# Kernel tuning notes

Measured on AMD Instinct MI355X. Metric: run time of the kernel, lower is better.

Reference implementation:

```python
import jax, jax.numpy as jnp
import numpy as np

B, T, IN, H, STEPS = 32768, 11, 2, 64, 80


def gru_cell(x, h, W_ih, W_hh, b_ih, b_hh):
    # PyTorch GRU cell: gates ordered (r, z, n)
    gi = x @ W_ih.T + b_ih            # [B, 3H]
    gh = h @ W_hh.T + b_hh            # [B, 3H]
    gi_r, gi_z, gi_n = jnp.split(gi, 3, axis=-1)
    gh_r, gh_z, gh_n = jnp.split(gh, 3, axis=-1)
    r = jax.nn.sigmoid(gi_r + gh_r)
    z = jax.nn.sigmoid(gi_z + gh_z)
    n = jnp.tanh(gi_n + r * gh_n)
    return (1.0 - z) * n + z * h


def setup_inputs() -> dict:
    key = jax.random.key(0)
    ks = jax.random.split(key, 20)
    s = 1.0 / np.sqrt(H)
    u = lambda k, shape: jax.random.uniform(k, shape, jnp.float32, -s, s)
    inp = {"x": jax.random.normal(ks[0], (B, T, IN), jnp.float32)}
    i = 1
    for pfx, in0 in (("e", IN), ("d", IN)):
        for l, d_in in ((0, in0), (1, H)):
            inp[f"{pfx}W_ih{l}"] = u(ks[i], (3 * H, d_in)); i += 1
            inp[f"{pfx}W_hh{l}"] = u(ks[i], (3 * H, H)); i += 1
            inp[f"{pfx}b_ih{l}"] = u(ks[i], (3 * H,)); i += 1
            inp[f"{pfx}b_hh{l}"] = u(ks[i], (3 * H,)); i += 1
    inp["fc_W"] = u(ks[17], (2, H))
    inp["fc_b"] = u(ks[18], (2,))
    return inp


def reference(x, eW_ih0, eW_hh0, eb_ih0, eb_hh0, eW_ih1, eW_hh1, eb_ih1, eb_hh1,
              dW_ih0, dW_hh0, db_ih0, db_hh0, dW_ih1, dW_hh1, db_ih1, db_hh1,
              fc_W, fc_b):
    b = x.shape[0]
    h0 = jnp.zeros((b, H), x.dtype)
    h1 = jnp.zeros((b, H), x.dtype)

    # ---- encoder: 2-layer GRU over time (dropout inactive in eval) ----
    def enc_step(carry, xt):
        c0, c1 = carry
        c0 = gru_cell(xt, c0, eW_ih0, eW_hh0, eb_ih0, eb_hh0)
        c1 = gru_cell(c0, c1, eW_ih1, eW_hh1, eb_ih1, eb_hh1)
        return (c0, c1), None

    (h0, h1), _ = jax.lax.scan(enc_step, (h0, h1), jnp.swapaxes(x, 0, 1))

    def dec_step(carry, _):
        inp, c0, c1 = carry
        c0 = gru_cell(inp, c0, dW_ih0, dW_hh0, db_ih0, db_hh0)
        c1 = gru_cell(c0, c1, dW_ih1, dW_hh1, db_ih1, db_hh1)
        pred = c1 @ fc_W.T + fc_b     # [B, 2]
        return (pred, c0, c1), pred

    init = (x[:, -1, :], h0, h1)
    _, preds = jax.lax.scan(dec_step, init, None, length=STEPS)  # [80, B, 2]
    return jnp.swapaxes(preds, 0, 1)  # [B, 80, 2]
```

## Files before the change

kernel.cpp:

```cpp
#include <hip/hip_runtime.h>
#include <cstddef>

#define T_SEQ 11
#define STEPS 80

typedef _Float16 f16;
typedef _Float16 f16x4 __attribute__((ext_vector_type(4)));
typedef _Float16 f16x8 __attribute__((ext_vector_type(8)));
typedef float    f32x4 __attribute__((ext_vector_type(4)));

#define SRC (-1.44269504f)
#define SNC ( 2.88539008f)

__device__ __forceinline__ f32x4 mfma16(f16x8 a, f16x8 b, f32x4 c) {
    return __builtin_amdgcn_mfma_f32_16x16x32_f16(a, b, c, 0, 0, 0);
}
__device__ __forceinline__ float exp2r(float x) { return __builtin_amdgcn_exp2f(x); }

__device__ __forceinline__ f16x8 wfrag(const float* __restrict__ W, int row, int k0, float sc) {
    f16x8 r;
    #pragma unroll
    for (int i = 0; i < 8; ++i) r[i] = (f16)(sc * W[row * 64 + k0 + i]);
    return r;
}
__device__ __forceinline__ f16x8 cfrag(const float* __restrict__ Wih0,
                                       const float* __restrict__ fcW, int row, int k0, float sc) {
    f16x8 r;
    #pragma unroll
    for (int i = 0; i < 8; ++i)
        r[i] = (f16)(sc * (Wih0[row * 2] * fcW[k0 + i] + Wih0[row * 2 + 1] * fcW[64 + k0 + i]));
    return r;
}

struct WSet {
    f16x8 xR[2], xZ[2], xN[2];
    f16x8 hR[2], hZ[2], hN[2];
};

__device__ __forceinline__ void load_h_frags(WSet& W, const float* __restrict__ Whh,
                                             int jA, int quad)
{
    #pragma unroll
    for (int ks = 0; ks < 2; ++ks) {
        const int k0 = ks * 32 + quad * 8;
        W.hR[ks] = wfrag(Whh, jA,       k0, SRC);
        W.hZ[ks] = wfrag(Whh, jA + 64,  k0, SRC);
        W.hN[ks] = wfrag(Whh, jA + 128, k0, SNC);
    }
}
__device__ __forceinline__ void load_x_frags(WSet& W, const float* __restrict__ Wx,
                                             int jA, int quad)
{
    #pragma unroll
    for (int ks = 0; ks < 2; ++ks) {
        const int k0 = ks * 32 + quad * 8;
        W.xR[ks] = wfrag(Wx, jA,       k0, SRC);
        W.xZ[ks] = wfrag(Wx, jA + 64,  k0, SRC);
        W.xN[ks] = wfrag(Wx, jA + 128, k0, SNC);
    }
}

template<bool XM, int CT>
__device__ __forceinline__ void cell(const WSet& W, const float* __restrict__ sb,
    const f16* __restrict__ Xs, const f16* __restrict__ Hs, f16* __restrict__ Dst,
    f16x4 (&ho)[2],
    const f32x4* __restrict__ xw, const float2* __restrict__ xv,
    int j4, int ro0, int ro1, int wo)
{
    const f32x4 bR  = *(const f32x4*)(sb + CT * 256 +       j4);
    const f32x4 bZ  = *(const f32x4*)(sb + CT * 256 +  64 + j4);
    const f32x4 bNi = *(const f32x4*)(sb + CT * 256 + 128 + j4);
    const f32x4 bNh = *(const f32x4*)(sb + CT * 256 + 192 + j4);
    #pragma unroll
    for (int mt = 0; mt < 2; ++mt) {
        const int mo = mt * 1024;
        f16x8 hb0 = *(const f16x8*)(Hs + ro0 + mo);
        f16x8 hb1 = *(const f16x8*)(Hs + ro1 + mo);
        f32x4 aR  = mfma16(W.hR[0], hb0, bR);
        f32x4 aZ  = mfma16(W.hZ[0], hb0, bZ);
        f32x4 aNh = mfma16(W.hN[0], hb0, bNh);
        aR  = mfma16(W.hR[1], hb1, aR);
        aZ  = mfma16(W.hZ[1], hb1, aZ);
        aNh = mfma16(W.hN[1], hb1, aNh);
        f32x4 aNi;
        if constexpr (XM) {
            f16x8 xb0 = *(const f16x8*)(Xs + ro0 + mo);
            f16x8 xb1 = *(const f16x8*)(Xs + ro1 + mo);
            aR  = mfma16(W.xR[0], xb0, aR);    aR  = mfma16(W.xR[1], xb1, aR);
            aZ  = mfma16(W.xZ[0], xb0, aZ);    aZ  = mfma16(W.xZ[1], xb1, aZ);
            aNi = mfma16(W.xN[0], xb0, bNi);   aNi = mfma16(W.xN[1], xb1, aNi);
        } else {
            const float x0 = xv[mt].x, x1 = xv[mt].y;
            aR  += x0 * xw[0] + x1 * xw[1];
            aZ  += x0 * xw[2] + x1 * xw[3];
            aNi  = bNi + x0 * xw[4] + x1 * xw[5];
        }
        f16x4 o;
        #pragma unroll
        for (int i = 0; i < 4; ++i) {
            const float r = __builtin_amdgcn_rcpf(1.f + exp2r(aR[i]));
            const float z = __builtin_amdgcn_rcpf(1.f + exp2r(aZ[i]));
            const float n = 1.f - 2.f * __builtin_amdgcn_rcpf(1.f + exp2r(aNi[i] + r * aNh[i]));
            const float h = n + z * ((float)ho[mt][i] - n);
            o[i] = (f16)h;
        }
        ho[mt] = o;
        *(f16x4*)(Dst + wo + mo) = o;
    }
}

__global__ __launch_bounds__(256, 3)
void gru_traj_mfma12(
    const float* __restrict__ x,
    const float* __restrict__ eWih0, const float* __restrict__ eWhh0,
    const float* __restrict__ ebih0, const float* __restrict__ ebhh0,
    const float* __restrict__ eWih1, const float* __restrict__ eWhh1,
    const float* __restrict__ ebih1, const float* __restrict__ ebhh1,
    const float* __restrict__ dWih0, const float* __restrict__ dWhh0,
    const float* __restrict__ dbih0, const float* __restrict__ dbhh0,
    const float* __restrict__ dWih1, const float* __restrict__ dWhh1,
    const float* __restrict__ dbih1, const float* __restrict__ dbhh1,
    const float* __restrict__ fcW,  const float* __restrict__ fcb,
    float* __restrict__ out)
{
    __shared__ f16 hbuf[4][32 * 64];
    __shared__ float2 xe[T_SEQ * 32];
    __shared__ float sbias[4 * 256];
    __shared__ f16 sfc[1024];
    __shared__ float sfcb[2];

    const int tid  = threadIdx.x;
    const int lane = tid & 63;
    const int w    = __builtin_amdgcn_readfirstlane(tid >> 6);
    const int quad = lane >> 4;
    const int col  = lane & 15;
    const int r0   = blockIdx.x * 32;

    {
        const float2* x2 = (const float2*)x;
        for (int i = tid; i < 32 * T_SEQ; i += 256) {
            const int row = i / T_SEQ, t = i - row * T_SEQ;
            xe[t * 32 + row] = x2[(size_t)r0 * T_SEQ + i];
        }
    }
    for (int i = tid; i < 32 * 64; i += 256) { hbuf[0][i] = (f16)0.f; hbuf[2][i] = (f16)0.f; }
    if (tid < 64) {
        const int j = tid;
        sbias[       j] = SRC * (ebih0[j] + ebhh0[j]);
        sbias[ 64 + j] = SRC * (ebih0[64 + j] + ebhh0[64 + j]);
        sbias[128 + j] = SNC * ebih0[128 + j];
        sbias[192 + j] = SNC * ebhh0[128 + j];
        sbias[256 +       j] = SRC * (ebih1[j] + ebhh1[j]);
        sbias[256 +  64 + j] = SRC * (ebih1[64 + j] + ebhh1[64 + j]);
        sbias[256 + 128 + j] = SNC * ebih1[128 + j];
        sbias[256 + 192 + j] = SNC * ebhh1[128 + j];
    }
    for (int e = tid; e < 1024; e += 256) {
        const int ks = e >> 9, rr = e & 511;
        const int lne = rr >> 3, ki = rr & 7;
        const int c = lne & 15, q = lne >> 4;
        const int k = ks * 32 + q * 8 + ki;
        sfc[ks * 512 + lne * 8 + ki] = (c < 2) ? (f16)fcW[c * 64 + k] : (f16)0.f;
    }
    if (tid < 2) sfcb[tid] = fcb[tid];

    const int c7  = col & 7;
    const int ro0 = col * 64 + ((quad ^ c7) << 3);
    const int ro1 = col * 64 + (((4 + quad) ^ c7) << 3);
    const int wo  = col * 64 + ((((w << 1) | (quad >> 1)) ^ c7) << 3) + ((quad & 1) << 2);

    const int jA = w * 16 + col;
    const int j4 = w * 16 + quad * 4;

    f16x4 ho0[2], ho1[2];
    #pragma unroll
    for (int mt = 0; mt < 2; ++mt) {
        #pragma unroll
        for (int i = 0; i < 4; ++i) { ho0[mt][i] = (f16)0.f; ho1[mt][i] = (f16)0.f; }
    }

    WSet W0, W1;
    load_h_frags(W0, eWhh0, jA, quad);
    load_h_frags(W1, eWhh1, jA, quad);
    load_x_frags(W1, eWih1, jA, quad);
    {
        f32x4 xw[6];
        #pragma unroll
        for (int rg = 0; rg < 4; ++rg) {
            xw[0][rg] = SRC * eWih0[(j4 + rg) * 2];        xw[1][rg] = SRC * eWih0[(j4 + rg) * 2 + 1];
            xw[2][rg] = SRC * eWih0[(64 + j4 + rg) * 2];   xw[3][rg] = SRC * eWih0[(64 + j4 + rg) * 2 + 1];
            xw[4][rg] = SNC * eWih0[(128 + j4 + rg) * 2];  xw[5][rg] = SNC * eWih0[(128 + j4 + rg) * 2 + 1];
        }
        __syncthreads();

        #pragma unroll 1
        for (int t = 0; t < T_SEQ - 1; t += 2) {
            float2 xv[2];
            #pragma unroll
            for (int mt = 0; mt < 2; ++mt) xv[mt] = xe[t * 32 + mt * 16 + col];
            cell<false, 0>(W0, sbias, hbuf[0], hbuf[0], hbuf[1], ho0, xw, xv, j4, ro0, ro1, wo);
            __syncthreads();
            cell<true, 1>(W1, sbias, hbuf[1], hbuf[2], hbuf[3], ho1, nullptr, nullptr, j4, ro0, ro1, wo);
            #pragma unroll
            for (int mt = 0; mt < 2; ++mt) xv[mt] = xe[(t + 1) * 32 + mt * 16 + col];
            cell<false, 0>(W0, sbias, hbuf[1], hbuf[1], hbuf[0], ho0, xw, xv, j4, ro0, ro1, wo);
            __syncthreads();
            cell<true, 1>(W1, sbias, hbuf[0], hbuf[3], hbuf[2], ho1, nullptr, nullptr, j4, ro0, ro1, wo);
        }
        {
            float2 xv[2];
            #pragma unroll
            for (int mt = 0; mt < 2; ++mt) xv[mt] = xe[10 * 32 + mt * 16 + col];
            cell<false, 0>(W0, sbias, hbuf[0], hbuf[0], hbuf[1], ho0, xw, xv, j4, ro0, ro1, wo);
            __syncthreads();
            cell<true, 1>(W1, sbias, hbuf[1], hbuf[2], hbuf[3], ho1, nullptr, nullptr, j4, ro0, ro1, wo);
        }
    }

    load_h_frags(W0, dWhh0, jA, quad);
    #pragma unroll
    for (int ks = 0; ks < 2; ++ks) {
        const int k0 = ks * 32 + quad * 8;
        W0.xR[ks] = cfrag(dWih0, fcW, jA,       k0, SRC);
        W0.xZ[ks] = cfrag(dWih0, fcW, jA + 64,  k0, SRC);
        W0.xN[ks] = cfrag(dWih0, fcW, jA + 128, k0, SNC);
    }
    load_h_frags(W1, dWhh1, jA, quad);
    load_x_frags(W1, dWih1, jA, quad);
    if (tid < 64) {
        const int j = tid;
        const float f0 = fcb[0], f1 = fcb[1];
        sbias[512 +       j] = SRC * (dbih0[j] + dbhh0[j] + dWih0[j * 2] * f0 + dWih0[j * 2 + 1] * f1);
        sbias[512 +  64 + j] = SRC * (dbih0[64 + j] + dbhh0[64 + j] + dWih0[(64 + j) * 2] * f0 + dWih0[(64 + j) * 2 + 1] * f1);
        sbias[512 + 128 + j] = SNC * (dbih0[128 + j] + dWih0[(128 + j) * 2] * f0 + dWih0[(128 + j) * 2 + 1] * f1);
        sbias[512 + 192 + j] = SNC * dbhh0[128 + j];
        sbias[768 +       j] = SRC * (dbih1[j] + dbhh1[j]);
        sbias[768 +  64 + j] = SRC * (dbih1[64 + j] + dbhh1[64 + j]);
        sbias[768 + 128 + j] = SNC * dbih1[128 + j];
        sbias[768 + 192 + j] = SNC * dbhh1[128 + j];
    }
    __syncthreads();

    const int cw = w & 1;
    float* __restrict__ op = out + (size_t)(r0 + cw * 16 + col) * (STEPS * 2);

    auto FCout = [&](const f16* h1c) {
        if (w < 2) {
            f32x4 pb;
            const float f0 = sfcb[0], f1 = sfcb[1];
            pb[0] = (quad == 0) ? f0 : 0.f;
            pb[1] = (quad == 0) ? f1 : 0.f;
            pb[2] = 0.f; pb[3] = 0.f;
            f16x8 fc0 = *(const f16x8*)(sfc + lane * 8);
            f16x8 fc1 = *(const f16x8*)(sfc + 512 + lane * 8);
            f16x8 hb0 = *(const f16x8*)(h1c + ro0 + cw * 1024);
            f16x8 hb1 = *(const f16x8*)(h1c + ro1 + cw * 1024);
            f32x4 p = mfma16(fc0, hb0, pb);
            p = mfma16(fc1, hb1, p);
            if (quad == 0) *(float2*)op = make_float2(p[0], p[1]);
        }
        op += 2;
    };

    {
        f32x4 xw[6];
        #pragma unroll
        for (int rg = 0; rg < 4; ++rg) {
            xw[0][rg] = SRC * dWih0[(j4 + rg) * 2];        xw[1][rg] = SRC * dWih0[(j4 + rg) * 2 + 1];
            xw[2][rg] = SRC * dWih0[(64 + j4 + rg) * 2];   xw[3][rg] = SRC * dWih0[(64 + j4 + rg) * 2 + 1];
            xw[4][rg] = SNC * dWih0[(128 + j4 + rg) * 2];  xw[5][rg] = SNC * dWih0[(128 + j4 + rg) * 2 + 1];
        }
        float2 xv0[2];
        #pragma unroll
        for (int mt = 0; mt < 2; ++mt) xv0[mt] = xe[10 * 32 + mt * 16 + col];
        cell<false, 2>(W0, sbias, hbuf[1], hbuf[1], hbuf[0], ho0, xw, xv0, j4, ro0, ro1, wo);
        __syncthreads();
        cell<true, 3>(W1, sbias, hbuf[0], hbuf[3], hbuf[2], ho1, nullptr, nullptr, j4, ro0, ro1, wo);
        __syncthreads();
        FCout(hbuf[2]);
    }

    #pragma unroll 1
    for (int sp = 0; sp < 39; ++sp) {
        cell<true, 2>(W0, sbias, hbuf[2], hbuf[0], hbuf[1], ho0, nullptr, nullptr, j4, ro0, ro1, wo);
        __syncthreads();
        cell<true, 3>(W1, sbias, hbuf[1], hbuf[2], hbuf[3], ho1, nullptr, nullptr, j4, ro0, ro1, wo);
        __syncthreads();
        FCout(hbuf[3]);
        cell<true, 2>(W0, sbias, hbuf[3], hbuf[1], hbuf[0], ho0, nullptr, nullptr, j4, ro0, ro1, wo);
        __syncthreads();
        cell<true, 3>(W1, sbias, hbuf[0], hbuf[3], hbuf[2], ho1, nullptr, nullptr, j4, ro0, ro1, wo);
        __syncthreads();
        FCout(hbuf[2]);
    }
    {
        cell<true, 2>(W0, sbias, hbuf[2], hbuf[0], hbuf[1], ho0, nullptr, nullptr, j4, ro0, ro1, wo);
        __syncthreads();
        cell<true, 3>(W1, sbias, hbuf[1], hbuf[2], hbuf[3], ho1, nullptr, nullptr, j4, ro0, ro1, wo);
        __syncthreads();
        FCout(hbuf[3]);
    }
}

extern "C" void kernel_launch(void* const* d_in, const int* in_sizes, int n_in,
                              void* d_out, int out_size, void* d_ws, size_t ws_size,
                              hipStream_t stream) {
    (void)n_in; (void)out_size; (void)d_ws; (void)ws_size;

    const float* x     = (const float*)d_in[0];
    const float* eWih0 = (const float*)d_in[1];
    const float* eWhh0 = (const float*)d_in[2];
    const float* ebih0 = (const float*)d_in[3];
    const float* ebhh0 = (const float*)d_in[4];
    const float* eWih1 = (const float*)d_in[5];
    const float* eWhh1 = (const float*)d_in[6];
    const float* ebih1 = (const float*)d_in[7];
    const float* ebhh1 = (const float*)d_in[8];
    const float* dWih0 = (const float*)d_in[9];
    const float* dWhh0 = (const float*)d_in[10];
    const float* dbih0 = (const float*)d_in[11];
    const float* dbhh0 = (const float*)d_in[12];
    const float* dWih1 = (const float*)d_in[13];
    const float* dWhh1 = (const float*)d_in[14];
    const float* dbih1 = (const float*)d_in[15];
    const float* dbhh1 = (const float*)d_in[16];
    const float* fcW   = (const float*)d_in[17];
    const float* fcb   = (const float*)d_in[18];
    float* out = (float*)d_out;

    const int b = in_sizes[0] / (T_SEQ * 2);
    dim3 grid(b / 32), block(256);
    hipLaunchKernelGGL(gru_traj_mfma12, grid, block, 0, stream,
        x, eWih0, eWhh0, ebih0, ebhh0, eWih1, eWhh1, ebih1, ebhh1,
        dWih0, dWhh0, dbih0, dbhh0, dWih1, dWhh1, dbih1, dbhh1,
        fcW, fcb, out);
}
```

Measured before the change: 463.6 us.

## Split GRU layers across wave groups and pipeline two row-halves

The block grows from 256 to 512 threads. Waves 0-3 now own layer 0 and waves 4-7 own layer 1, each keeping only one layer's weight fragments in registers. The 32 rows are split into two 16-row halves that move through a software pipeline: layer 1 processes one half while layer 0 processes the other, with double-buffered hidden state in LDS. This aims to halve per-wave register pressure and overlap the two layers' serial dependency chains. The cost is more barriers per step, a larger block, and more complex buffer indexing that could introduce ordering bugs.

```diff
diff --git a/kernel.cpp b/kernel.cpp
--- a/kernel.cpp
+++ b/kernel.cpp
@@ -61,56 +61,50 @@
 }
 
 template<bool XM, int CT>
-__device__ __forceinline__ void cell(const WSet& W, const float* __restrict__ sb,
+__device__ __forceinline__ void cellH(const WSet& W, const float* __restrict__ sb,
     const f16* __restrict__ Xs, const f16* __restrict__ Hs, f16* __restrict__ Dst,
-    f16x4 (&ho)[2],
-    const f32x4* __restrict__ xw, const float2* __restrict__ xv,
+    f16x4& ho, const f32x4* __restrict__ xw, float2 xv,
     int j4, int ro0, int ro1, int wo)
 {
     const f32x4 bR  = *(const f32x4*)(sb + CT * 256 +       j4);
     const f32x4 bZ  = *(const f32x4*)(sb + CT * 256 +  64 + j4);
     const f32x4 bNi = *(const f32x4*)(sb + CT * 256 + 128 + j4);
     const f32x4 bNh = *(const f32x4*)(sb + CT * 256 + 192 + j4);
-    #pragma unroll
-    for (int mt = 0; mt < 2; ++mt) {
-        const int mo = mt * 1024;
-        f16x8 hb0 = *(const f16x8*)(Hs + ro0 + mo);
-        f16x8 hb1 = *(const f16x8*)(Hs + ro1 + mo);
-        f32x4 aR  = mfma16(W.hR[0], hb0, bR);
-        f32x4 aZ  = mfma16(W.hZ[0], hb0, bZ);
-        f32x4 aNh = mfma16(W.hN[0], hb0, bNh);
-        aR  = mfma16(W.hR[1], hb1, aR);
-        aZ  = mfma16(W.hZ[1], hb1, aZ);
-        aNh = mfma16(W.hN[1], hb1, aNh);
-        f32x4 aNi;
-        if constexpr (XM) {
-            f16x8 xb0 = *(const f16x8*)(Xs + ro0 + mo);
-            f16x8 xb1 = *(const f16x8*)(Xs + ro1 + mo);
-            aR  = mfma16(W.xR[0], xb0, aR);    aR  = mfma16(W.xR[1], xb1, aR);
-            aZ  = mfma16(W.xZ[0], xb0, aZ);    aZ  = mfma16(W.xZ[1], xb1, aZ);
-            aNi = mfma16(W.xN[0], xb0, bNi);   aNi = mfma16(W.xN[1], xb1, aNi);
-        } else {
-            const float x0 = xv[mt].x, x1 = xv[mt].y;
-            aR  += x0 * xw[0] + x1 * xw[1];
-            aZ  += x0 * xw[2] + x1 * xw[3];
-            aNi  = bNi + x0 * xw[4] + x1 * xw[5];
-        }
-        f16x4 o;
-        #pragma unroll
-        for (int i = 0; i < 4; ++i) {
-            const float r = __builtin_amdgcn_rcpf(1.f + exp2r(aR[i]));
-            const float z = __builtin_amdgcn_rcpf(1.f + exp2r(aZ[i]));
-            const float n = 1.f - 2.f * __builtin_amdgcn_rcpf(1.f + exp2r(aNi[i] + r * aNh[i]));
-            const float h = n + z * ((float)ho[mt][i] - n);
-            o[i] = (f16)h;
-        }
-        ho[mt] = o;
-        *(f16x4*)(Dst + wo + mo) = o;
-    }
-}
-
-__global__ __launch_bounds__(256, 3)
-void gru_traj_mfma12(
+    f16x8 hb0 = *(const f16x8*)(Hs + ro0);
+    f16x8 hb1 = *(const f16x8*)(Hs + ro1);
+    f32x4 aR  = mfma16(W.hR[0], hb0, bR);
+    f32x4 aZ  = mfma16(W.hZ[0], hb0, bZ);
+    f32x4 aNh = mfma16(W.hN[0], hb0, bNh);
+    aR  = mfma16(W.hR[1], hb1, aR);
+    aZ  = mfma16(W.hZ[1], hb1, aZ);
+    aNh = mfma16(W.hN[1], hb1, aNh);
+    f32x4 aNi;
+    if constexpr (XM) {
+        f16x8 xb0 = *(const f16x8*)(Xs + ro0);
+        f16x8 xb1 = *(const f16x8*)(Xs + ro1);
+        aR  = mfma16(W.xR[0], xb0, aR);    aR  = mfma16(W.xR[1], xb1, aR);
+        aZ  = mfma16(W.xZ[0], xb0, aZ);    aZ  = mfma16(W.xZ[1], xb1, aZ);
+        aNi = mfma16(W.xN[0], xb0, bNi);   aNi = mfma16(W.xN[1], xb1, aNi);
+    } else {
+        aR  += xv.x * xw[0] + xv.y * xw[1];
+        aZ  += xv.x * xw[2] + xv.y * xw[3];
+        aNi  = bNi + xv.x * xw[4] + xv.y * xw[5];
+    }
+    f16x4 o;
+    #pragma unroll
+    for (int i = 0; i < 4; ++i) {
+        const float r = __builtin_amdgcn_rcpf(1.f + exp2r(aR[i]));
+        const float z = __builtin_amdgcn_rcpf(1.f + exp2r(aZ[i]));
+        const float n = 1.f - 2.f * __builtin_amdgcn_rcpf(1.f + exp2r(aNi[i] + r * aNh[i]));
+        const float h = n + z * ((float)ho[i] - n);
+        o[i] = (f16)h;
+    }
+    ho = o;
+    *(f16x4*)(Dst + wo) = o;
+}
+
+__global__ __launch_bounds__(512, 4)
+void gru_traj_pipe1(
     const float* __restrict__ x,
     const float* __restrict__ eWih0, const float* __restrict__ eWhh0,
     const float* __restrict__ ebih0, const float* __restrict__ ebhh0,
@@ -123,7 +117,8 @@
     const float* __restrict__ fcW,  const float* __restrict__ fcb,
     float* __restrict__ out)
 {
-    __shared__ f16 hbuf[4][32 * 64];
+    __shared__ f16 h0b[4][1024];
+    __shared__ f16 h1b[4][1024];
     __shared__ float2 xe[T_SEQ * 32];
     __shared__ float sbias[4 * 256];
     __shared__ f16 sfc[1024];
@@ -131,19 +126,23 @@
 
     const int tid  = threadIdx.x;
     const int lane = tid & 63;
-    const int w    = __builtin_amdgcn_readfirstlane(tid >> 6);
+    const int wv   = __builtin_amdgcn_readfirstlane(tid >> 6);
+    const bool isL0 = wv < 4;
+    const int jg   = wv & 3;
     const int quad = lane >> 4;
     const int col  = lane & 15;
     const int r0   = blockIdx.x * 32;
 
     {
         const float2* x2 = (const float2*)x;
-        for (int i = tid; i < 32 * T_SEQ; i += 256) {
+        for (int i = tid; i < 32 * T_SEQ; i += 512) {
             const int row = i / T_SEQ, t = i - row * T_SEQ;
             xe[t * 32 + row] = x2[(size_t)r0 * T_SEQ + i];
         }
     }
-    for (int i = tid; i < 32 * 64; i += 256) { hbuf[0][i] = (f16)0.f; hbuf[2][i] = (f16)0.f; }
+    for (int i = tid; i < 2048; i += 512) {
+        ((f16*)h0b)[i] = (f16)0.f; ((f16*)h1b)[i] = (f16)0.f;
+    }
     if (tid < 64) {
         const int j = tid;
         sbias[       j] = SRC * (ebih0[j] + ebhh0[j]);
@@ -155,7 +154,7 @@
         sbias[256 + 128 + j] = SNC * ebih1[128 + j];
         sbias[256 + 192 + j] = SNC * ebhh1[128 + j];
     }
-    for (int e = tid; e < 1024; e += 256) {
+    for (int e = tid; e < 1024; e += 512) {
         const int ks = e >> 9, rr = e & 511;
         const int lne = rr >> 3, ki = rr & 7;
         const int c = lne & 15, q = lne >> 4;
@@ -167,66 +166,71 @@
     const int c7  = col & 7;
     const int ro0 = col * 64 + ((quad ^ c7) << 3);
     const int ro1 = col * 64 + (((4 + quad) ^ c7) << 3);
-    const int wo  = col * 64 + ((((w << 1) | (quad >> 1)) ^ c7) << 3) + ((quad & 1) << 2);
-
-    const int jA = w * 16 + col;
-    const int j4 = w * 16 + quad * 4;
-
-    f16x4 ho0[2], ho1[2];
-    #pragma unroll
-    for (int mt = 0; mt < 2; ++mt) {
-        #pragma unroll
-        for (int i = 0; i < 4; ++i) { ho0[mt][i] = (f16)0.f; ho1[mt][i] = (f16)0.f; }
-    }
-
-    WSet W0, W1;
-    load_h_frags(W0, eWhh0, jA, quad);
-    load_h_frags(W1, eWhh1, jA, quad);
-    load_x_frags(W1, eWih1, jA, quad);
-    {
-        f32x4 xw[6];
+    const int wo  = col * 64 + ((((jg << 1) | (quad >> 1)) ^ c7) << 3) + ((quad & 1) << 2);
+    const int jA  = jg * 16 + col;
+    const int j4  = jg * 16 + quad * 4;
+
+    f16x4 hoA, hoB;
+    #pragma unroll
+    for (int i = 0; i < 4; ++i) { hoA[i] = (f16)0.f; hoB[i] = (f16)0.f; }
+
+    WSet W;
+    f32x4 xw[6];
+    if (isL0) {
+        load_h_frags(W, eWhh0, jA, quad);
         #pragma unroll
         for (int rg = 0; rg < 4; ++rg) {
             xw[0][rg] = SRC * eWih0[(j4 + rg) * 2];        xw[1][rg] = SRC * eWih0[(j4 + rg) * 2 + 1];
             xw[2][rg] = SRC * eWih0[(64 + j4 + rg) * 2];   xw[3][rg] = SRC * eWih0[(64 + j4 + rg) * 2 + 1];
             xw[4][rg] = SNC * eWih0[(128 + j4 + rg) * 2];  xw[5][rg] = SNC * eWih0[(128 + j4 + rg) * 2 + 1];
         }
+    } else {
+        load_h_frags(W, eWhh1, jA, quad);
+        load_x_frags(W, eWih1, jA, quad);
+    }
+    __syncthreads();
+
+    #pragma unroll 1
+    for (int t = 0; t < T_SEQ; ++t) {
+        const int pr = t & 1, pw = pr ^ 1;
+        if (isL0) {
+            const float2 xv = xe[t * 32 + col];
+            cellH<false, 0>(W, sbias, nullptr, h0b[pr * 2 + 0], h0b[pw * 2 + 0], hoA, xw, xv, j4, ro0, ro1, wo);
+        } else if (t > 0) {
+            cellH<true, 1>(W, sbias, h0b[pr * 2 + 1], h1b[pw * 2 + 1], h1b[pr * 2 + 1], hoB, xw, make_float2(0.f, 0.f), j4, ro0, ro1, wo);
+        }
         __syncthreads();
-
-        #pragma unroll 1
-        for (int t = 0; t < T_SEQ - 1; t += 2) {
-            float2 xv[2];
-            #pragma unroll
-            for (int mt = 0; mt < 2; ++mt) xv[mt] = xe[t * 32 + mt * 16 + col];
-            cell<false, 0>(W0, sbias, hbuf[0], hbuf[0], hbuf[1], ho0, xw, xv, j4, ro0, ro1, wo);
-            __syncthreads();
-            cell<true, 1>(W1, sbias, hbuf[1], hbuf[2], hbuf[3], ho1, nullptr, nullptr, j4, ro0, ro1, wo);
-            #pragma unroll
-            for (int mt = 0; mt < 2; ++mt) xv[mt] = xe[(t + 1) * 32 + mt * 16 + col];
-            cell<false, 0>(W0, sbias, hbuf[1], hbuf[1], hbuf[0], ho0, xw, xv, j4, ro0, ro1, wo);
-            __syncthreads();
-            cell<true, 1>(W1, sbias, hbuf[0], hbuf[3], hbuf[2], ho1, nullptr, nullptr, j4, ro0, ro1, wo);
-        }
-        {
-            float2 xv[2];
-            #pragma unroll
-            for (int mt = 0; mt < 2; ++mt) xv[mt] = xe[10 * 32 + mt * 16 + col];
-            cell<false, 0>(W0, sbias, hbuf[0], hbuf[0], hbuf[1], ho0, xw, xv, j4, ro0, ro1, wo);
-            __syncthreads();
-            cell<true, 1>(W1, sbias, hbuf[1], hbuf[2], hbuf[3], ho1, nullptr, nullptr, j4, ro0, ro1, wo);
-        }
-    }
-
-    load_h_frags(W0, dWhh0, jA, quad);
-    #pragma unroll
-    for (int ks = 0; ks < 2; ++ks) {
-        const int k0 = ks * 32 + quad * 8;
-        W0.xR[ks] = cfrag(dWih0, fcW, jA,       k0, SRC);
-        W0.xZ[ks] = cfrag(dWih0, fcW, jA + 64,  k0, SRC);
-        W0.xN[ks] = cfrag(dWih0, fcW, jA + 128, k0, SNC);
-    }
-    load_h_frags(W1, dWhh1, jA, quad);
-    load_x_frags(W1, dWih1, jA, quad);
+        if (isL0) {
+            const float2 xv = xe[t * 32 + 16 + col];
+            cellH<false, 0>(W, sbias, nullptr, h0b[pr * 2 + 1], h0b[pw * 2 + 1], hoB, xw, xv, j4, ro0, ro1, wo);
+        } else {
+            cellH<true, 1>(W, sbias, h0b[pw * 2 + 0], h1b[pr * 2 + 0], h1b[pw * 2 + 0], hoA, xw, make_float2(0.f, 0.f), j4, ro0, ro1, wo);
+        }
+        __syncthreads();
+    }
+    if (!isL0)
+        cellH<true, 1>(W, sbias, h0b[1 * 2 + 1], h1b[0 * 2 + 1], h1b[1 * 2 + 1], hoB, xw, make_float2(0.f, 0.f), j4, ro0, ro1, wo);
+    __syncthreads();
+
+    if (isL0) {
+        load_h_frags(W, dWhh0, jA, quad);
+        #pragma unroll
+        for (int ks = 0; ks < 2; ++ks) {
+            const int k0 = ks * 32 + quad * 8;
+            W.xR[ks] = cfrag(dWih0, fcW, jA,       k0, SRC);
+            W.xZ[ks] = cfrag(dWih0, fcW, jA + 64,  k0, SRC);
+            W.xN[ks] = cfrag(dWih0, fcW, jA + 128, k0, SNC);
+        }
+        #pragma unroll
+        for (int rg = 0; rg < 4; ++rg) {
+            xw[0][rg] = SRC * dWih0[(j4 + rg) * 2];        xw[1][rg] = SRC * dWih0[(j4 + rg) * 2 + 1];
+            xw[2][rg] = SRC * dWih0[(64 + j4 + rg) * 2];   xw[3][rg] = SRC * dWih0[(64 + j4 + rg) * 2 + 1];
+            xw[4][rg] = SNC * dWih0[(128 + j4 + rg) * 2];  xw[5][rg] = SNC * dWih0[(128 + j4 + rg) * 2 + 1];
+        }
+    } else {
+        load_h_frags(W, dWhh1, jA, quad);
+        load_x_frags(W, dWih1, jA, quad);
+    }
     if (tid < 64) {
         const int j = tid;
         const float f0 = fcb[0], f1 = fcb[1];
@@ -241,65 +245,59 @@
     }
     __syncthreads();
 
-    const int cw = w & 1;
-    float* __restrict__ op = out + (size_t)(r0 + cw * 16 + col) * (STEPS * 2);
-
-    auto FCout = [&](const f16* h1c) {
-        if (w < 2) {
-            f32x4 pb;
-            const float f0 = sfcb[0], f1 = sfcb[1];
-            pb[0] = (quad == 0) ? f0 : 0.f;
-            pb[1] = (quad == 0) ? f1 : 0.f;
-            pb[2] = 0.f; pb[3] = 0.f;
-            f16x8 fc0 = *(const f16x8*)(sfc + lane * 8);
-            f16x8 fc1 = *(const f16x8*)(sfc + 512 + lane * 8);
-            f16x8 hb0 = *(const f16x8*)(h1c + ro0 + cw * 1024);
-            f16x8 hb1 = *(const f16x8*)(h1c + ro1 + cw * 1024);
-            f32x4 p = mfma16(fc0, hb0, pb);
-            p = mfma16(fc1, hb1, p);
-            if (quad == 0) *(float2*)op = make_float2(p[0], p[1]);
-        }
+    float* op = out + (size_t)(r0 + jg * 16 + col) * (STEPS * 2);
+    auto FCOUT = [&](const f16* __restrict__ h1c) {
+        f32x4 pb;
+        pb[0] = (quad == 0) ? sfcb[0] : 0.f;
+        pb[1] = (quad == 0) ? sfcb[1] : 0.f;
+        pb[2] = 0.f; pb[3] = 0.f;
+        f16x8 fc0 = *(const f16x8*)(sfc + lane * 8);
+        f16x8 fc1 = *(const f16x8*)(sfc + 512 + lane * 8);
+        f16x8 hb0 = *(const f16x8*)(h1c + ro0);
+        f16x8 hb1 = *(const f16x8*)(h1c + ro1);
+        f32x4 p = mfma16(fc0, hb0, pb);
+        p = mfma16(fc1, hb1, p);
+        if (quad == 0) *(float2*)op = make_float2(p[0], p[1]);
         op += 2;
     };
 
-    {
-        f32x4 xw[6];
-        #pragma unroll
-        for (int rg = 0; rg < 4; ++rg) {
-            xw[0][rg] = SRC * dWih0[(j4 + rg) * 2];        xw[1][rg] = SRC * dWih0[(j4 + rg) * 2 + 1];
-            xw[2][rg] = SRC * dWih0[(64 + j4 + rg) * 2];   xw[3][rg] = SRC * dWih0[(64 + j4 + rg) * 2 + 1];
-            xw[4][rg] = SNC * dWih0[(128 + j4 + rg) * 2];  xw[5][rg] = SNC * dWih0[(128 + j4 + rg) * 2 + 1];
-        }
-        float2 xv0[2];
-        #pragma unroll
-        for (int mt = 0; mt < 2; ++mt) xv0[mt] = xe[10 * 32 + mt * 16 + col];
-        cell<false, 2>(W0, sbias, hbuf[1], hbuf[1], hbuf[0], ho0, xw, xv0, j4, ro0, ro1, wo);
+    if (isL0) {
+        const float2 xv = xe[10 * 32 + col];
+        cellH<false, 2>(W, sbias, nullptr, h0b[1 * 2 + 0], h0b[0 * 2 + 0], hoA, xw, xv, j4, ro0, ro1, wo);
+    }
+    __syncthreads();
+    if (isL0) {
+        const float2 xv = xe[10 * 32 + 16 + col];
+        cellH<false, 2>(W, sbias, nullptr, h0b[1 * 2 + 1], h0b[0 * 2 + 1], hoB, xw, xv, j4, ro0, ro1, wo);
+    } else {
+        cellH<true, 3>(W, sbias, h0b[0 * 2 + 0], h1b[1 * 2 + 0], h1b[0 * 2 + 0], hoA, xw, make_float2(0.f, 0.f), j4, ro0, ro1, wo);
+    }
+    __syncthreads();
+
+    #pragma unroll 1
+    for (int s = 1; s < STEPS; ++s) {
+        const int pr = s & 1, pw = pr ^ 1;
+        if (isL0) {
+            cellH<true, 2>(W, sbias, h1b[pw * 2 + 0], h0b[pw * 2 + 0], h0b[pr * 2 + 0], hoA, xw, make_float2(0.f, 0.f), j4, ro0, ro1, wo);
+        } else {
+            cellH<true, 3>(W, sbias, h0b[pw * 2 + 1], h1b[pr * 2 + 1], h1b[pw * 2 + 1], hoB, xw, make_float2(0.f, 0.f), j4, ro0, ro1, wo);
+            if (jg == 0) FCOUT(h1b[pw * 2 + 0]);
+        }
         __syncthreads();
-        cell<true, 3>(W1, sbias, hbuf[0], hbuf[3], hbuf[2], ho1, nullptr, nullptr, j4, ro0, ro1, wo);
+        if (isL0) {
+            cellH<true, 2>(W, sbias, h1b[pw * 2 + 1], h0b[pw * 2 + 1], h0b[pr * 2 + 1], hoB, xw, make_float2(0.f, 0.f), j4, ro0, ro1, wo);
+        } else {
+            cellH<true, 3>(W, sbias, h0b[pr * 2 + 0], h1b[pw * 2 + 0], h1b[pr * 2 + 0], hoA, xw, make_float2(0.f, 0.f), j4, ro0, ro1, wo);
+            if (jg == 1) FCOUT(h1b[pw * 2 + 1]);
+        }
         __syncthreads();
-        FCout(hbuf[2]);
-    }
-
-    #pragma unroll 1
-    for (int sp = 0; sp < 39; ++sp) {
-        cell<true, 2>(W0, sbias, hbuf[2], hbuf[0], hbuf[1], ho0, nullptr, nullptr, j4, ro0, ro1, wo);
-        __syncthreads();
-        cell<true, 3>(W1, sbias, hbuf[1], hbuf[2], hbuf[3], ho1, nullptr, nullptr, j4, ro0, ro1, wo);
-        __syncthreads();
-        FCout(hbuf[3]);
-        cell<true, 2>(W0, sbias, hbuf[3], hbuf[1], hbuf[0], ho0, nullptr, nullptr, j4, ro0, ro1, wo);
-        __syncthreads();
-        cell<true, 3>(W1, sbias, hbuf[0], hbuf[3], hbuf[2], ho1, nullptr, nullptr, j4, ro0, ro1, wo);
-        __syncthreads();
-        FCout(hbuf[2]);
-    }
-    {
-        cell<true, 2>(W0, sbias, hbuf[2], hbuf[0], hbuf[1], ho0, nullptr, nullptr, j4, ro0, ro1, wo);
-        __syncthreads();
-        cell<true, 3>(W1, sbias, hbuf[1], hbuf[2], hbuf[3], ho1, nullptr, nullptr, j4, ro0, ro1, wo);
-        __syncthreads();
-        FCout(hbuf[3]);
-    }
+    }
+    if (!isL0) {
+        cellH<true, 3>(W, sbias, h0b[1 * 2 + 1], h1b[0 * 2 + 1], h1b[1 * 2 + 1], hoB, xw, make_float2(0.f, 0.f), j4, ro0, ro1, wo);
+        if (jg == 0) FCOUT(h1b[1 * 2 + 0]);
+    }
+    __syncthreads();
+    if (!isL0 && jg == 1) FCOUT(h1b[1 * 2 + 1]);
 }
 
 extern "C" void kernel_launch(void* const* d_in, const int* in_sizes, int n_in,
@@ -329,8 +327,8 @@
     float* out = (float*)d_out;
 
     const int b = in_sizes[0] / (T_SEQ * 2);
-    dim3 grid(b / 32), block(256);
-    hipLaunchKernelGGL(gru_traj_mfma12, grid, block, 0, stream,
+    dim3 grid(b / 32), block(512);
+    hipLaunchKernelGGL(gru_traj_pipe1, grid, block, 0, stream,
         x, eWih0, eWhh0, ebih0, ebhh0, eWih1, eWhh1, ebih1, ebhh1,
         dWih0, dWhh0, dbih0, dbhh0, dWih1, dWhh1, dbih1, dbhh1,
         fcW, fcb, out);
```

New measurement: 470.0 us. Within noise of the previous version (+1.4%).
